# Kernel optimization log

Measured on AMD Instinct MI355X. Metric: run time of the kernel, lower is better.

Reference implementation:

```python
import jax, jax.numpy as jnp
import numpy as np

N, C, H, W = 64, 512, 32, 32
HID, NCLS = 240, 10


def setup_inputs() -> dict:
    key = jax.random.key(0)
    ks = jax.random.split(key, 6)
    d = {
        "x": jax.random.normal(ks[0], (N, C, H, W), jnp.float32),
        "bn1_g": jnp.ones((C,), jnp.float32),
        "bn1_b": jnp.zeros((C,), jnp.float32),
        "bn1_m": jnp.zeros((C,), jnp.float32),
        "bn1_v": jnp.ones((C,), jnp.float32),
        "conv1_w": jax.random.normal(ks[1], (C, C, 3, 3), jnp.float32) * 0.02,
        "bn2_g": jnp.ones((C,), jnp.float32),
        "bn2_b": jnp.zeros((C,), jnp.float32),
        "bn2_m": jnp.zeros((C,), jnp.float32),
        "bn2_v": jnp.ones((C,), jnp.float32),
        "conv2_w": jax.random.normal(ks[2], (C, C, 3, 3), jnp.float32) * 0.02,
        "fc1_w": jax.random.normal(ks[3], (HID, C), jnp.float32) * 0.05,
        "fc1_b": jnp.zeros((HID,), jnp.float32),
        "fc2_w": jax.random.normal(ks[4], (NCLS, HID), jnp.float32) * 0.05,
        "fc2_b": jnp.zeros((NCLS,), jnp.float32),
    }
    return d


def _bn(x, g, b, m, v, eps=1e-5):
    # eval-mode BatchNorm2d, NCHW
    inv = g / jnp.sqrt(v + eps)
    return x * inv[None, :, None, None] + (b - m * inv)[None, :, None, None]


def _conv3(x, w):
    return jax.lax.conv_general_dilated(
        x, w, window_strides=(1, 1), padding="SAME",
        dimension_numbers=("NCHW", "OIHW", "NCHW"))


def _probe(feat, fc1_w, fc1_b, fc2_w, fc2_b):
    # Global_Avg_Flatten -> Linear -> Softplus(beta=5) -> Linear
    g = feat.mean(axis=(2, 3))                       # (N, C)
    h = jax.nn.softplus(5.0 * (g @ fc1_w.T + fc1_b)) / 5.0  # (N, HID)
    return h @ fc2_w.T + fc2_b                       # (N, NCLS)


def _get_mask(feat, fc1_w, fc1_b, fc2_w, fc2_b):
    # eval branch: sum of top-1 + top-2 logits, grad wrt (detached) feat
    feat_sg = jax.lax.stop_gradient(feat)

    def logit_sum(f_):
        logits = _probe(f_, fc1_w, fc1_b, fc2_w, fc2_b)
        idx = jax.lax.top_k(logits, 2)[1]            # (N, 2) int indices
        return jnp.take_along_axis(logits, idx, axis=1).sum()

    g = jax.grad(logit_sum)(feat_sg)                 # (N, C, H, W)
    # adaptive_avg_pool2d(.,1)*H*W == spatial sum
    s = g.sum(axis=(2, 3))                           # (N, C)
    m = jax.nn.softmax(s, axis=1) * 2.0
    return m[:, :, None, None]


def reference(x, bn1_g, bn1_b, bn1_m, bn1_v, conv1_w,
              bn2_g, bn2_b, bn2_m, bn2_v, conv2_w,
              fc1_w, fc1_b, fc2_w, fc2_b):
    out1 = jax.nn.relu(_bn(x, bn1_g, bn1_b, bn1_m, bn1_v))  # equalInOut path
    mask = _get_mask(out1, fc1_w, fc1_b, fc2_w, fc2_b)
    pred_probe = _probe(out1, fc1_w, fc1_b, fc2_w, fc2_b)
    masked = out1 * mask
    h = jax.nn.relu(_bn(_conv3(masked, conv1_w), bn2_g, bn2_b, bn2_m, bn2_v))
    h = _conv3(h, conv2_w)
    out = x + h
    return (out, pred_probe)
```

## Files before the change

kernel.cpp:

```cpp
#include <hip/hip_runtime.h>
#include <stdint.h>

typedef __bf16 bf16x8 __attribute__((ext_vector_type(8)));
typedef float f32x4v __attribute__((ext_vector_type(4)));

typedef __attribute__((address_space(1))) const void gconst_t;
typedef __attribute__((address_space(3))) void lds_t;

#define GLL16(gp, sp) __builtin_amdgcn_global_load_lds((gconst_t*)(uintptr_t)(gp), (lds_t*)(uintptr_t)(sp), 16, 0, 0)

__device__ __forceinline__ unsigned short f2bf(float f) {
  unsigned int u = __float_as_uint(f);
  u = (u + 0x7FFFu + ((u >> 16) & 1u)) >> 16;
  return (unsigned short)u;
}
__device__ __forceinline__ float bf2f(unsigned int b) {
  return __uint_as_float(b << 16);
}

#define SPP 1156

__global__ __launch_bounds__(512) void bnprep(
    const float* __restrict__ g1, const float* __restrict__ b1,
    const float* __restrict__ m1, const float* __restrict__ v1,
    const float* __restrict__ g2, const float* __restrict__ b2,
    const float* __restrict__ m2, const float* __restrict__ v2,
    float* __restrict__ bnp) {
  int t = threadIdx.x;
  float i1 = g1[t] * rsqrtf(v1[t] + 1e-5f);
  bnp[t] = i1;
  bnp[512 + t] = b1[t] - m1[t] * i1;
  float i2 = g2[t] * rsqrtf(v2[t] + 1e-5f);
  bnp[1024 + t] = i2;
  bnp[1536 + t] = b2[t] - m2[t] * i2;
}

__global__ __launch_bounds__(256) void ring_zero(unsigned short* __restrict__ Ap,
                                                 unsigned short* __restrict__ Hp) {
  const int n = blockIdx.y;
  const int p = blockIdx.x * 4 + (threadIdx.x >> 6);
  const int lane = threadIdx.x & 63;
  int y, x;
  if (p < 34) { y = 0; x = p; }
  else if (p < 68) { y = 33; x = p - 34; }
  else if (p < 100) { y = p - 67; x = 0; }
  else { y = p - 99; x = 33; }
  const uint4 z = {0u, 0u, 0u, 0u};
  const size_t off = ((size_t)((n * 34 + y) * 34 + x)) * 512 + lane * 8;
  *(uint4*)(Ap + off) = z;
  *(uint4*)(Hp + off) = z;
}

__global__ __launch_bounds__(256) void wtrans(const float* __restrict__ w1, const float* __restrict__ w2,
                                              unsigned short* __restrict__ w1t, unsigned short* __restrict__ w2t) {
  unsigned e = blockIdx.x * 256u + threadIdx.x;
  if (e >= 4718592u) return;
  const float* w = (e < 2359296u) ? w1 : w2;
  unsigned short* o = (e < 2359296u) ? w1t : w2t;
  unsigned r = (e < 2359296u) ? e : (e - 2359296u);
  unsigned ci = r & 511u, co = (r >> 9) & 511u, tt = r >> 18;
  o[r] = f2bf(w[(co * 512u + ci) * 9u + tt]);
}

__global__ __launch_bounds__(256) void bn1_relu_stage(const float* __restrict__ x, const float* __restrict__ bnp,
                                                      unsigned short* __restrict__ Ap, float* __restrict__ partial) {
  int bid = blockIdx.x;
  int n = bid >> 6, ciblk = (bid >> 3) & 7, yblk = bid & 7;
  int ci0 = ciblk * 64, y0 = yblk * 4;
  int t = threadIdx.x;
  __shared__ __align__(16) float vals[64 * 128];
  __shared__ float ivs[64], bbs[64];
  if (t < 64) { ivs[t] = bnp[ci0 + t]; bbs[t] = bnp[512 + ci0 + t]; }
  __syncthreads();
#pragma unroll
  for (int i = 0; i < 8; ++i) {
    int f4 = i * 256 + t;
    int cil = f4 >> 5, xq = f4 & 31;
    const float* src = x + ((size_t)(n * 512 + ci0 + cil)) * 1024 + y0 * 32 + xq * 4;
    f32x4v v = *(const f32x4v*)src;
    float iv = ivs[cil], bb = bbs[cil];
    f32x4v r;
    r[0] = fmaxf(fmaf(v[0], iv, bb), 0.f);
    r[1] = fmaxf(fmaf(v[1], iv, bb), 0.f);
    r[2] = fmaxf(fmaf(v[2], iv, bb), 0.f);
    r[3] = fmaxf(fmaf(v[3], iv, bb), 0.f);
    *(f32x4v*)&vals[cil * 128 + xq * 4] = r;
  }
  __syncthreads();
  {
    int cil = t >> 2, q = t & 3;
    float s = 0.f;
#pragma unroll
    for (int j = 0; j < 32; ++j) s += vals[cil * 128 + q * 32 + j];
    s += __shfl_xor(s, 1);
    s += __shfl_xor(s, 2);
    if (q == 0) partial[((size_t)n * 512 + ci0 + cil) * 8 + yblk] = s;
  }
  {
    int yx = t >> 1, half = t & 1;
    int y = y0 + (yx >> 5), xx = yx & 31;
    unsigned short* dp = Ap + ((size_t)((n * 34 + y + 1) * 34 + (xx + 1))) * 512 + ci0 + half * 32;
    unsigned wrd[16];
#pragma unroll
    for (int j = 0; j < 16; ++j) {
      unsigned lo = f2bf(vals[(half * 32 + 2 * j) * 128 + yx]);
      unsigned hi = f2bf(vals[(half * 32 + 2 * j + 1) * 128 + yx]);
      wrd[j] = lo | (hi << 16);
    }
#pragma unroll
    for (int k = 0; k < 4; ++k) {
      uint4 u;
      u.x = wrd[k * 4]; u.y = wrd[k * 4 + 1]; u.z = wrd[k * 4 + 2]; u.w = wrd[k * 4 + 3];
      *(uint4*)(dp + k * 8) = u;
    }
  }
}

__global__ __launch_bounds__(256) void probe_mask(const float* __restrict__ partial,
                                                  const float* __restrict__ fc1w, const float* __restrict__ fc1b,
                                                  const float* __restrict__ fc2w, const float* __restrict__ fc2b,
                                                  float* __restrict__ maskp, float* __restrict__ probeout) {
  int n = blockIdx.x, t = threadIdx.x;
  int lane = t & 63, wv = t >> 6;
  __shared__ float gl[512], sl[512], zl[240], hl[240], dzl[240], logl[10], red[4];
  __shared__ int idx2[2];
  for (int c = t; c < 512; c += 256) {
    const float* pp = partial + ((size_t)n * 512 + c) * 8;
    float s = 0.f;
#pragma unroll
    for (int j = 0; j < 8; ++j) s += pp[j];
    gl[c] = s * (1.f / 1024.f);
  }
  __syncthreads();
  if (t < 240) {
    float z = fc1b[t];
    const float* wr = fc1w + t * 512;
    for (int c = 0; c < 512; ++c) z = fmaf(gl[c], wr[c], z);
    zl[t] = z;
    float u = 5.f * z;
    float sp = (u > 20.f) ? u : log1pf(expf(u));
    hl[t] = sp * 0.2f;
  }
  __syncthreads();
  if (t < 10) {
    float L = fc2b[t];
    const float* wr = fc2w + t * 240;
    for (int h = 0; h < 240; ++h) L = fmaf(hl[h], wr[h], L);
    logl[t] = L;
    probeout[n * 10 + t] = L;
  }
  __syncthreads();
  if (t == 0) {
    float b1v = -1e30f, b2v = -1e30f; int i1 = 0, i2 = 0;
    for (int j = 0; j < 10; ++j) {
      float v = logl[j];
      if (v > b1v) { b2v = b1v; i2 = i1; b1v = v; i1 = j; }
      else if (v > b2v) { b2v = v; i2 = j; }
    }
    idx2[0] = i1; idx2[1] = i2;
  }
  __syncthreads();
  if (t < 240) {
    float dh = fc2w[idx2[0] * 240 + t] + fc2w[idx2[1] * 240 + t];
    float u = 5.f * zl[t];
    float sg = 1.f / (1.f + expf(-u));
    dzl[t] = dh * sg;
  }
  __syncthreads();
  for (int c = t; c < 512; c += 256) {
    float s = 0.f;
    for (int h = 0; h < 240; ++h) s = fmaf(dzl[h], fc1w[h * 512 + c], s);
    sl[c] = s;
  }
  __syncthreads();
  float m = fmaxf(sl[t], sl[t + 256]);
#pragma unroll
  for (int o = 32; o > 0; o >>= 1) m = fmaxf(m, __shfl_xor(m, o));
  if (lane == 0) red[wv] = m;
  __syncthreads();
  float mx = fmaxf(fmaxf(red[0], red[1]), fmaxf(red[2], red[3]));
  float e0 = expf(sl[t] - mx), e1 = expf(sl[t + 256] - mx);
  float sum = e0 + e1;
#pragma unroll
  for (int o = 32; o > 0; o >>= 1) sum += __shfl_xor(sum, o);
  __syncthreads();
  if (lane == 0) red[wv] = sum;
  __syncthreads();
  float inv = 2.f / (red[0] + red[1] + red[2] + red[3]);
  maskp[(size_t)n * 512 + t] = e0 * inv;
  maskp[(size_t)n * 512 + t + 256] = e1 * inv;
}

__global__ __launch_bounds__(256) void apply_mask(unsigned short* __restrict__ Ap, const float* __restrict__ maskp) {
  int n = blockIdx.y;
  size_t off = (size_t)n * (SPP * 512) + (size_t)blockIdx.x * 2048 + threadIdx.x * 8;
  int ci0 = (int)(threadIdx.x * 8) & 511;
  uint4 v = *(uint4*)(Ap + off);
  const float* mp = maskp + n * 512 + ci0;
  unsigned r0, r1;
  r0 = f2bf(bf2f(v.x & 0xFFFFu) * mp[0]); r1 = f2bf(bf2f(v.x >> 16) * mp[1]); v.x = r0 | (r1 << 16);
  r0 = f2bf(bf2f(v.y & 0xFFFFu) * mp[2]); r1 = f2bf(bf2f(v.y >> 16) * mp[3]); v.y = r0 | (r1 << 16);
  r0 = f2bf(bf2f(v.z & 0xFFFFu) * mp[4]); r1 = f2bf(bf2f(v.z >> 16) * mp[5]); v.z = r0 | (r1 << 16);
  r0 = f2bf(bf2f(v.w & 0xFFFFu) * mp[6]); r1 = f2bf(bf2f(v.w >> 16) * mp[7]); v.w = r0 | (r1 << 16);
  *(uint4*)(Ap + off) = v;
}

#define RD_A(QM, BOF) do {                                                    \
  const char* _p0 = ldsb + (BOF) + (QM) * 8192 + aRd0;                        \
  const char* _p1 = ldsb + (BOF) + (QM) * 8192 + aRd1;                        \
  _Pragma("unroll") for (int mi = 0; mi < 4; ++mi) {                          \
    a[mi][0] = *(const bf16x8*)(_p0 + mi * 2048);                             \
    a[mi][1] = *(const bf16x8*)(_p1 + mi * 2048); }                           \
} while (0)

#define RD_B(QN, BOF) do {                                                    \
  const char* _p0 = ldsb + (BOF) + (QN) * 4096 + bRd0;                        \
  const char* _p1 = ldsb + (BOF) + (QN) * 4096 + bRd1;                        \
  _Pragma("unroll") for (int ni = 0; ni < 2; ++ni) {                          \
    b[QN][ni][0] = *(const bf16x8*)(_p0 + ni * 2048);                         \
    b[QN][ni][1] = *(const bf16x8*)(_p1 + ni * 2048); }                       \
} while (0)

#define ST_A(BOF, H, AP) do {                                                 \
  GLL16((AP) + aOff[H][0], ldsb + (BOF) + (H) * 16384 + tb);                  \
  GLL16((AP) + aOff[H][1], ldsb + (BOF) + (H) * 16384 + 8192 + tb);           \
} while (0)

#define ST_B(BOF, H, BP) do {                                                 \
  GLL16((BP) + bOff[H][0], ldsb + 65536 + (BOF) + (H) * 16384 + tb);          \
  GLL16((BP) + bOff[H][1], ldsb + 65536 + (BOF) + (H) * 16384 + 8192 + tb);   \
} while (0)

#define MFMA_Q(QM, QN) do {                                                   \
  _Pragma("unroll") for (int mi = 0; mi < 4; ++mi)                            \
  _Pragma("unroll") for (int ni = 0; ni < 2; ++ni) {                          \
    acc[QM][QN][mi][ni] = __builtin_amdgcn_mfma_f32_16x16x32_bf16(            \
        a[mi][0], b[QN][ni][0], acc[QM][QN][mi][ni], 0, 0, 0);                \
    acc[QM][QN][mi][ni] = __builtin_amdgcn_mfma_f32_16x16x32_bf16(            \
        a[mi][1], b[QN][ni][1], acc[QM][QN][mi][ni], 0, 0, 0); }              \
} while (0)

#define BARR __builtin_amdgcn_s_barrier()
#define LGKM0 do { asm volatile("s_waitcnt lgkmcnt(0)" ::: "memory");         \
                   __builtin_amdgcn_sched_barrier(0); } while (0)
#define VM4 asm volatile("s_waitcnt vmcnt(4)" ::: "memory")
#define PRIO1 __builtin_amdgcn_s_setprio(1)
#define PRIO0 __builtin_amdgcn_s_setprio(0)

#define TILE_PTRS(KT, APn, BPn)                                               \
  const unsigned short *APn, *BPn;                                            \
  { int _kt = (KT); int _tap = _kt >> 3; int _kin = (_kt & 7) << 6;           \
    int _dy = (_tap * 11) >> 5; int _dx = _tap - _dy * 3;                     \
    APn = Ag + (size_t)(_dy * 34 + _dx) * 512 + _kin;                         \
    BPn = Wt + (size_t)_tap * 262144 + _kin; }

template <int MODE>
__global__ __launch_bounds__(512, 2) void conv256(
    const unsigned short* __restrict__ Ain,
    const unsigned short* __restrict__ Wt,
    const float* __restrict__ bnp,
    unsigned short* __restrict__ Hout,
    const float* __restrict__ xres,
    float* __restrict__ outp) {
  __shared__ __align__(16) char ldsb[131072];

  const int t = threadIdx.x;
  const int lane = t & 63;
  const int wv = t >> 6;
  const int wm = wv >> 2;
  const int wn = wv & 3;

  const int bid = blockIdx.x;
  const int swz = (bid & 7) * 64 + (bid >> 3);
  const int nt = swz & 1, mt = swz >> 1;
  const int n = mt >> 2, yblk = mt & 3;
  const int co0 = nt * 256;

  const unsigned short* Ag = Ain + (size_t)n * (SPP * 512);

  int aOff[2][2], bOff[2][2];
#pragma unroll
  for (int i = 0; i < 2; ++i) {
    const int c = i * 512 + t;
    const int lr = c >> 3;
    const int kq = (c & 7) ^ (lr & 7);
#pragma unroll
    for (int h = 0; h < 2; ++h) {
      aOff[h][i] = ((yblk * 8 + h * 4 + (lr >> 5)) * 34 + (lr & 31)) * 512 + kq * 8;
      bOff[h][i] = (co0 + h * 128 + lr) * 512 + kq * 8;
    }
  }
  const int tb = t * 16;
  const int k0 = (((lane >> 4) ^ (lane & 7)) << 4);
  const int aRd0 = wm * 16384 + (lane & 15) * 128 + k0;
  const int aRd1 = aRd0 ^ 64;
  const int bRd0 = 65536 + (wn >> 1) * 16384 + (((wn & 1) << 6) + (lane & 15)) * 128 + k0;
  const int bRd1 = bRd0 ^ 64;

  bf16x8 a[4][2];
  bf16x8 b[2][2][2];
  f32x4v acc[2][2][4][2];
  const f32x4v zero = {0.f, 0.f, 0.f, 0.f};
#pragma unroll
  for (int qm = 0; qm < 2; ++qm)
#pragma unroll
    for (int qn = 0; qn < 2; ++qn)
#pragma unroll
      for (int mi = 0; mi < 4; ++mi)
#pragma unroll
        for (int ni = 0; ni < 2; ++ni) acc[qm][qn][mi][ni] = zero;

  {
    TILE_PTRS(0, ap0, bp0);
    TILE_PTRS(1, ap1p, bp1p);
    ST_B(0, 0, bp0); ST_B(0, 1, bp0);
    ST_A(0, 0, ap0); ST_A(0, 1, ap0);
    ST_B(32768, 0, bp1p); ST_B(32768, 1, bp1p);
    (void)ap1p;
    VM4;
    BARR;
  }

  for (int it = 0; it < 36; ++it) {
    const int u = 2 * it;
    TILE_PTRS(u + 1, ap1, bp1);
    (void)bp1;
    int kt2 = u + 2; if (kt2 > 71) kt2 = 71;
    int kt3 = u + 3; if (kt3 > 71) kt3 = 71;
    TILE_PTRS(kt2, ap2, bp2);
    TILE_PTRS(kt3, ap3, bp3);
    (void)ap3;

    RD_A(0, 0); RD_B(0, 0);
    ST_A(32768, 0, ap1);
    BARR; LGKM0;
    PRIO1; MFMA_Q(0, 0); PRIO0;
    BARR;
    RD_B(1, 0);
    ST_A(32768, 1, ap1);
    BARR; LGKM0;
    PRIO1; MFMA_Q(0, 1); PRIO0;
    BARR;
    RD_A(1, 0);
    ST_B(0, 0, bp2);
    BARR; LGKM0;
    PRIO1; MFMA_Q(1, 1); PRIO0;
    BARR;
    ST_B(0, 1, bp2);
    BARR;
    PRIO1; MFMA_Q(1, 0); PRIO0;
    VM4;
    BARR;
    RD_A(0, 32768); RD_B(0, 32768);
    ST_A(0, 0, ap2);
    BARR; LGKM0;
    PRIO1; MFMA_Q(0, 0); PRIO0;
    BARR;
    RD_B(1, 32768);
    ST_A(0, 1, ap2);
    BARR; LGKM0;
    PRIO1; MFMA_Q(0, 1); PRIO0;
    BARR;
    RD_A(1, 32768);
    ST_B(32768, 0, bp3);
    BARR; LGKM0;
    PRIO1; MFMA_Q(1, 1); PRIO0;
    BARR;
    ST_B(32768, 1, bp3);
    BARR;
    PRIO1; MFMA_Q(1, 0); PRIO0;
    VM4;
    BARR;
  }
  asm volatile("s_waitcnt vmcnt(0)" ::: "memory");
  __syncthreads();

  if constexpr (MODE == 1) {
#pragma unroll
    for (int qn = 0; qn < 2; ++qn)
#pragma unroll
      for (int ni = 0; ni < 2; ++ni) {
        const int cog = co0 + wn * 64 + qn * 32 + ni * 16 + (lane & 15);
        const float iv = bnp[1024 + cog];
        const float bb = bnp[1536 + cog];
#pragma unroll
        for (int qm = 0; qm < 2; ++qm)
#pragma unroll
          for (int mi = 0; mi < 4; ++mi)
#pragma unroll
            for (int r = 0; r < 4; ++r) {
              const int row = wm * 128 + qm * 64 + mi * 16 + (lane >> 4) * 4 + r;
              const int y = yblk * 8 + (row >> 5), xx = row & 31;
              const float v = fmaxf(fmaf(acc[qm][qn][mi][ni][r], iv, bb), 0.f);
              Hout[((size_t)((n * 34 + y + 1) * 34 + (xx + 1))) * 512 + cog] = f2bf(v);
            }
      }
  } else {
    float* sm = (float*)ldsb;
    const int spat0 = yblk * 256;
#pragma unroll 1
    for (int h = 0; h < 4; ++h) {
      if (wn == h) {
#pragma unroll
        for (int qn = 0; qn < 2; ++qn)
#pragma unroll
          for (int ni = 0; ni < 2; ++ni)
#pragma unroll
            for (int qm = 0; qm < 2; ++qm)
#pragma unroll
              for (int mi = 0; mi < 4; ++mi)
#pragma unroll
                for (int r = 0; r < 4; ++r)
                  sm[(qn * 32 + ni * 16 + (lane & 15)) * 264 +
                     wm * 128 + qm * 64 + mi * 16 + (lane >> 4) * 4 + r] = acc[qm][qn][mi][ni][r];
      }
      __syncthreads();
#pragma unroll
      for (int j = 0; j < 8; ++j) {
        const int c = j * 512 + t;
        const int cc = c >> 6, px = (c & 63) * 4;
        f32x4v v = *(const f32x4v*)&sm[cc * 264 + px];
        const int cog = co0 + h * 64 + cc;
        const size_t o = ((size_t)(n * 512 + cog)) * 1024 + spat0 + px;
        const f32x4v xr = *(const f32x4v*)(xres + o);
        v = v + xr;
        *(f32x4v*)(outp + o) = v;
      }
      __syncthreads();
    }
  }
}

extern "C" void kernel_launch(void* const* d_in, const int* in_sizes, int n_in,
                              void* d_out, int out_size, void* d_ws, size_t ws_size,
                              hipStream_t stream) {
  (void)in_sizes; (void)n_in; (void)out_size; (void)ws_size;
  const float* x    = (const float*)d_in[0];
  const float* bn1g = (const float*)d_in[1];
  const float* bn1b = (const float*)d_in[2];
  const float* bn1m = (const float*)d_in[3];
  const float* bn1v = (const float*)d_in[4];
  const float* w1   = (const float*)d_in[5];
  const float* bn2g = (const float*)d_in[6];
  const float* bn2b = (const float*)d_in[7];
  const float* bn2m = (const float*)d_in[8];
  const float* bn2v = (const float*)d_in[9];
  const float* w2   = (const float*)d_in[10];
  const float* fc1w = (const float*)d_in[11];
  const float* fc1b = (const float*)d_in[12];
  const float* fc2w = (const float*)d_in[13];
  const float* fc2b = (const float*)d_in[14];

  float* out = (float*)d_out;
  float* probeo = out + (size_t)64 * 512 * 32 * 32;

  char* ws = (char*)d_ws;
  unsigned short* Ap  = (unsigned short*)(ws);
  unsigned short* Hp  = (unsigned short*)(ws + 75759616);
  unsigned short* W1t = (unsigned short*)(ws + 151519232);
  unsigned short* W2t = (unsigned short*)(ws + 156237824);
  float* partial      = (float*)(ws + 160956416);
  float* maskp        = (float*)(ws + 162004992);
  float* bnp          = (float*)(ws + 162136064);

  bnprep<<<1, 512, 0, stream>>>(bn1g, bn1b, bn1m, bn1v, bn2g, bn2b, bn2m, bn2v, bnp);
  ring_zero<<<dim3(33, 64), 256, 0, stream>>>(Ap, Hp);
  wtrans<<<18432, 256, 0, stream>>>(w1, w2, W1t, W2t);
  bn1_relu_stage<<<4096, 256, 0, stream>>>(x, bnp, Ap, partial);
  probe_mask<<<64, 256, 0, stream>>>(partial, fc1w, fc1b, fc2w, fc2b, maskp, probeo);
  apply_mask<<<dim3(289, 64), 256, 0, stream>>>(Ap, maskp);
  conv256<1><<<512, 512, 0, stream>>>(Ap, W1t, bnp, Hp, nullptr, nullptr);
  conv256<2><<<512, 512, 0, stream>>>(Hp, W2t, bnp, nullptr, x, out);
}
```

Baseline: 616.3 us.

## Reuse haloed input slab in LDS across all nine conv taps

Reorders the implicit-GEMM conv loop to iterate channel-chunk outer and tap inner, loading a haloed 8+2-row input slab into LDS once per 64-channel chunk and reading each tap's A tile from shifted LDS offsets. This cuts global/LDS A-tile loads by roughly nine times, and B (weights) moves to a triple buffer. LDS use grows to 144KB, and the A slab reload needs a full vmcnt(0) drain plus extra barriers at each chunk boundary. That could stall the pipeline, and bank conflicts from the new swizzle indexing are possible.

```diff
diff --git a/kernel.cpp b/kernel.cpp
--- a/kernel.cpp
+++ b/kernel.cpp
@@ -205,30 +205,41 @@
   *(uint4*)(Ap + off) = v;
 }
 
-#define RD_A(QM, BOF) do {                                                    \
-  const char* _p0 = ldsb + (BOF) + (QM) * 8192 + aRd0;                        \
-  const char* _p1 = ldsb + (BOF) + (QM) * 8192 + aRd1;                        \
-  _Pragma("unroll") for (int mi = 0; mi < 4; ++mi) {                          \
-    a[mi][0] = *(const bf16x8*)(_p0 + mi * 2048);                             \
-    a[mi][1] = *(const bf16x8*)(_p1 + mi * 2048); }                           \
-} while (0)
-
-#define RD_B(QN, BOF) do {                                                    \
-  const char* _p0 = ldsb + (BOF) + (QN) * 4096 + bRd0;                        \
-  const char* _p1 = ldsb + (BOF) + (QN) * 4096 + bRd1;                        \
+#define RD_A(QM, TAP) do {                                                    \
+  const int _c0 = ((((QM) * 2 + (TAP) / 3) * 34 + (TAP) % 3)) * 128;          \
+  const int _l0 = lterm[((((QM) * 2 + (TAP) / 3) * 34 + (TAP) % 3)) & 7];     \
+  const int _c1 = _c0 + 8704;                                                 \
+  const int _l1 = lterm[((((QM) * 2 + (TAP) / 3) * 34 + (TAP) % 3) + 4) & 7]; \
+  a[0][0] = *(const bf16x8*)(ldsAW + _c0 + _l0);                              \
+  a[0][1] = *(const bf16x8*)(ldsAW + _c0 + (_l0 ^ 64));                       \
+  a[1][0] = *(const bf16x8*)(ldsAW + _c0 + 2048 + _l0);                       \
+  a[1][1] = *(const bf16x8*)(ldsAW + _c0 + 2048 + (_l0 ^ 64));                \
+  a[2][0] = *(const bf16x8*)(ldsAW + _c1 + _l1);                              \
+  a[2][1] = *(const bf16x8*)(ldsAW + _c1 + (_l1 ^ 64));                       \
+  a[3][0] = *(const bf16x8*)(ldsAW + _c1 + 2048 + _l1);                       \
+  a[3][1] = *(const bf16x8*)(ldsAW + _c1 + 2048 + (_l1 ^ 64));                \
+} while (0)
+
+#define RD_B(QN, BUFR) do {                                                   \
+  const int _b0 = 49152 + (BUFR) * 32768 + (QN) * 4096 + bRdC;                \
   _Pragma("unroll") for (int ni = 0; ni < 2; ++ni) {                          \
-    b[QN][ni][0] = *(const bf16x8*)(_p0 + ni * 2048);                         \
-    b[QN][ni][1] = *(const bf16x8*)(_p1 + ni * 2048); }                       \
-} while (0)
-
-#define ST_A(BOF, H, AP) do {                                                 \
-  GLL16((AP) + aOff[H][0], ldsb + (BOF) + (H) * 16384 + tb);                  \
-  GLL16((AP) + aOff[H][1], ldsb + (BOF) + (H) * 16384 + 8192 + tb);           \
-} while (0)
-
-#define ST_B(BOF, H, BP) do {                                                 \
-  GLL16((BP) + bOff[H][0], ldsb + 65536 + (BOF) + (H) * 16384 + tb);          \
-  GLL16((BP) + bOff[H][1], ldsb + 65536 + (BOF) + (H) * 16384 + 8192 + tb);   \
+    b[QN][ni][0] = *(const bf16x8*)(ldsb + _b0 + ni * 2048);                  \
+    b[QN][ni][1] = *(const bf16x8*)(ldsb + (_b0 ^ 64) + ni * 2048); }         \
+} while (0)
+
+#define ST_B(BUFW, H, BP) do {                                                \
+  GLL16((BP) + bOff[H][0], ldsb + 49152 + (BUFW) * 32768 + (H) * 16384 + tb); \
+  GLL16((BP) + bOff[H][1],                                                    \
+        ldsb + 49152 + (BUFW) * 32768 + (H) * 16384 + 8192 + tb);             \
+} while (0)
+
+#define ST_A3(AP) do {                                                        \
+  GLL16((AP) + aSrc[0], ldsb + tb);                                           \
+  GLL16((AP) + aSrc[1], ldsb + 8192 + tb);                                    \
+  GLL16((AP) + aSrc[2], ldsb + 16384 + tb);                                   \
+  GLL16((AP) + aSrc[3], ldsb + 24576 + tb);                                   \
+  GLL16((AP) + aSrc[4], ldsb + 32768 + tb);                                   \
+  GLL16((AP) + aSrc[5], ldsb + 40960 + tb);                                   \
 } while (0)
 
 #define MFMA_Q(QM, QN) do {                                                   \
@@ -244,15 +255,44 @@
 #define LGKM0 do { asm volatile("s_waitcnt lgkmcnt(0)" ::: "memory");         \
                    __builtin_amdgcn_sched_barrier(0); } while (0)
 #define VM4 asm volatile("s_waitcnt vmcnt(4)" ::: "memory")
+#define VM0 asm volatile("s_waitcnt vmcnt(0)" ::: "memory")
 #define PRIO1 __builtin_amdgcn_s_setprio(1)
 #define PRIO0 __builtin_amdgcn_s_setprio(0)
 
-#define TILE_PTRS(KT, APn, BPn)                                               \
-  const unsigned short *APn, *BPn;                                            \
-  { int _kt = (KT); int _tap = _kt >> 3; int _kin = (_kt & 7) << 6;           \
-    int _dy = (_tap * 11) >> 5; int _dx = _tap - _dy * 3;                     \
-    APn = Ag + (size_t)(_dy * 34 + _dx) * 512 + _kin;                         \
-    BPn = Wt + (size_t)_tap * 262144 + _kin; }
+#define TAPSTEP(TAP) do {                                                     \
+  const unsigned short* _bp2;                                                 \
+  if ((TAP) <= 6)      _bp2 = Wt + (size_t)((TAP) + 2) * 262144 + k8 * 64;    \
+  else if ((TAP) == 7) _bp2 = (k8 < 7) ? Wt + (size_t)(k8 + 1) * 64           \
+                                       : Wt + (size_t)8 * 262144 + 7 * 64;    \
+  else                 _bp2 = (k8 < 7) ? Wt + 262144 + (size_t)(k8 + 1) * 64  \
+                                       : Wt + (size_t)8 * 262144 + 7 * 64;    \
+                                                                     \
+  RD_A(0, TAP); RD_B(0, (TAP) % 3);                                           \
+  ST_B(((TAP) + 2) % 3, 0, _bp2);                                             \
+  BARR; LGKM0;                                                                \
+  PRIO1; MFMA_Q(0, 0); PRIO0;                                                 \
+  BARR;                                                                       \
+                                                                     \
+  RD_B(1, (TAP) % 3);                                                         \
+  ST_B(((TAP) + 2) % 3, 1, _bp2);                                             \
+  BARR; LGKM0;                                                                \
+  PRIO1; MFMA_Q(0, 1); PRIO0;                                                 \
+  BARR;                                                                       \
+                                                                     \
+  RD_A(1, TAP);                                                               \
+  BARR; LGKM0;                                                                \
+  if ((TAP) < 8) {                                                            \
+    PRIO1; MFMA_Q(1, 1); MFMA_Q(1, 0); PRIO0;                                 \
+    VM4; BARR;                                                                \
+  } else {                                                                    \
+    PRIO1; MFMA_Q(1, 1); PRIO0;                                               \
+    BARR;                                                                     \
+    if (k8 < 7) { ST_A3(Ag + (size_t)(k8 + 1) * 64); }                        \
+    BARR;                                                                     \
+    PRIO1; MFMA_Q(1, 0); PRIO0;                                               \
+    VM0; BARR;                                                                \
+  }                                                                           \
+} while (0)
 
 template <int MODE>
 __global__ __launch_bounds__(512, 2) void conv256(
@@ -262,7 +302,7 @@
     unsigned short* __restrict__ Hout,
     const float* __restrict__ xres,
     float* __restrict__ outp) {
-  __shared__ __align__(16) char ldsb[131072];
+  __shared__ __align__(16) char ldsb[147456];
 
   const int t = threadIdx.x;
   const int lane = t & 63;
@@ -278,24 +318,31 @@
 
   const unsigned short* Ag = Ain + (size_t)n * (SPP * 512);
 
-  int aOff[2][2], bOff[2][2];
+  int bOff[2][2];
 #pragma unroll
   for (int i = 0; i < 2; ++i) {
     const int c = i * 512 + t;
     const int lr = c >> 3;
     const int kq = (c & 7) ^ (lr & 7);
 #pragma unroll
-    for (int h = 0; h < 2; ++h) {
-      aOff[h][i] = ((yblk * 8 + h * 4 + (lr >> 5)) * 34 + (lr & 31)) * 512 + kq * 8;
+    for (int h = 0; h < 2; ++h)
       bOff[h][i] = (co0 + h * 128 + lr) * 512 + kq * 8;
-    }
+  }
+  int aSrc[6];
+#pragma unroll
+  for (int r = 0; r < 6; ++r) {
+    const int s = r * 64 + (t >> 3);
+    const int kq = (t & 7) ^ (s & 7);
+    aSrc[r] = (yblk * 272 + s) * 512 + kq * 8;
   }
   const int tb = t * 16;
-  const int k0 = (((lane >> 4) ^ (lane & 7)) << 4);
-  const int aRd0 = wm * 16384 + (lane & 15) * 128 + k0;
-  const int aRd1 = aRd0 ^ 64;
-  const int bRd0 = 65536 + (wn >> 1) * 16384 + (((wn & 1) << 6) + (lane & 15)) * 128 + k0;
-  const int bRd1 = bRd0 ^ 64;
+  const int k0 = ((lane >> 4) ^ (lane & 7)) << 4;
+  int lterm[8];
+#pragma unroll
+  for (int m = 0; m < 8; ++m)
+    lterm[m] = (lane & 15) * 128 + (((lane >> 4) ^ ((m + (lane & 15)) & 7)) << 4);
+  const char* ldsAW = ldsb + wm * 17408;
+  const int bRdC = (wn >> 1) * 16384 + (((wn & 1) << 6) + (lane & 15)) * 128 + k0;
 
   bf16x8 a[4][2];
   bf16x8 b[2][2][2];
@@ -311,68 +358,18 @@
         for (int ni = 0; ni < 2; ++ni) acc[qm][qn][mi][ni] = zero;
 
   {
-    TILE_PTRS(0, ap0, bp0);
-    TILE_PTRS(1, ap1p, bp1p);
-    ST_B(0, 0, bp0); ST_B(0, 1, bp0);
-    ST_A(0, 0, ap0); ST_A(0, 1, ap0);
-    ST_B(32768, 0, bp1p); ST_B(32768, 1, bp1p);
-    (void)ap1p;
-    VM4;
-    BARR;
-  }
-
-  for (int it = 0; it < 36; ++it) {
-    const int u = 2 * it;
-    TILE_PTRS(u + 1, ap1, bp1);
-    (void)bp1;
-    int kt2 = u + 2; if (kt2 > 71) kt2 = 71;
-    int kt3 = u + 3; if (kt3 > 71) kt3 = 71;
-    TILE_PTRS(kt2, ap2, bp2);
-    TILE_PTRS(kt3, ap3, bp3);
-    (void)ap3;
-
-    RD_A(0, 0); RD_B(0, 0);
-    ST_A(32768, 0, ap1);
-    BARR; LGKM0;
-    PRIO1; MFMA_Q(0, 0); PRIO0;
-    BARR;
-    RD_B(1, 0);
-    ST_A(32768, 1, ap1);
-    BARR; LGKM0;
-    PRIO1; MFMA_Q(0, 1); PRIO0;
-    BARR;
-    RD_A(1, 0);
-    ST_B(0, 0, bp2);
-    BARR; LGKM0;
-    PRIO1; MFMA_Q(1, 1); PRIO0;
-    BARR;
-    ST_B(0, 1, bp2);
-    BARR;
-    PRIO1; MFMA_Q(1, 0); PRIO0;
-    VM4;
-    BARR;
-    RD_A(0, 32768); RD_B(0, 32768);
-    ST_A(0, 0, ap2);
-    BARR; LGKM0;
-    PRIO1; MFMA_Q(0, 0); PRIO0;
-    BARR;
-    RD_B(1, 32768);
-    ST_A(0, 1, ap2);
-    BARR; LGKM0;
-    PRIO1; MFMA_Q(0, 1); PRIO0;
-    BARR;
-    RD_A(1, 32768);
-    ST_B(32768, 0, bp3);
-    BARR; LGKM0;
-    PRIO1; MFMA_Q(1, 1); PRIO0;
-    BARR;
-    ST_B(32768, 1, bp3);
-    BARR;
-    PRIO1; MFMA_Q(1, 0); PRIO0;
-    VM4;
-    BARR;
-  }
-  asm volatile("s_waitcnt vmcnt(0)" ::: "memory");
+    ST_A3(Ag);
+    ST_B(0, 0, Wt); ST_B(0, 1, Wt);
+    ST_B(1, 0, Wt + 262144); ST_B(1, 1, Wt + 262144);
+    VM0; BARR;
+  }
+
+  for (int k8 = 0; k8 < 8; ++k8) {
+    TAPSTEP(0); TAPSTEP(1); TAPSTEP(2);
+    TAPSTEP(3); TAPSTEP(4); TAPSTEP(5);
+    TAPSTEP(6); TAPSTEP(7); TAPSTEP(8);
+  }
+  VM0;
   __syncthreads();
 
   if constexpr (MODE == 1) {
```

Measured after the change: 599.9 us. -2.7%, faster.
